# Kernel tuning notes

Measured on AMD Instinct MI355X. Metric: run time of the kernel, lower is better.

The kernel has to match this reference:

```python
import jax, jax.numpy as jnp
import numpy as np

N, F, H, C, CLS = 100000, 128, 4, 32, 2
E = 1600000
NEG_SLOPE = 0.2


def setup_inputs() -> dict:
    key = jax.random.key(0)
    ks = jax.random.split(key, 8)
    x = jax.random.normal(ks[0], (N, F), dtype=jnp.float32)
    edge_index = jax.random.randint(ks[1], (2, E), 0, N, dtype=jnp.int64)
    # GATConv params (PyG layout): lin weight [H*C, F], att vectors [H, C], bias [H*C]
    W_gat = jax.random.normal(ks[2], (H * C, F), dtype=jnp.float32) * (1.0 / np.sqrt(F))
    att_src = jax.random.normal(ks[3], (H, C), dtype=jnp.float32) * (1.0 / np.sqrt(C))
    att_dst = jax.random.normal(ks[4], (H, C), dtype=jnp.float32) * (1.0 / np.sqrt(C))
    b_gat = jnp.zeros((H * C,), dtype=jnp.float32)
    # final classifier Linear(H*C -> CLS)
    W_lin = jax.random.normal(ks[5], (CLS, H * C), dtype=jnp.float32) * (1.0 / np.sqrt(H * C))
    b_lin = jnp.zeros((CLS,), dtype=jnp.float32)
    return {"x": x, "edge_index": edge_index, "W_gat": W_gat, "att_src": att_src,
            "att_dst": att_dst, "b_gat": b_gat, "W_lin": W_lin, "b_lin": b_lin}


def _gat_conv(x, edge_index, W_gat, att_src, att_dst, b_gat):
    # add self loops (PyG default add_self_loops=True)
    loop = jnp.arange(N, dtype=edge_index.dtype)
    src = jnp.concatenate([edge_index[0], loop])  # [E+N]
    dst = jnp.concatenate([edge_index[1], loop])
    h = (x @ W_gat.T).reshape(N, H, C)            # [N, H, C]
    a_src = jnp.einsum('nhc,hc->nh', h, att_src)  # [N, H]
    a_dst = jnp.einsum('nhc,hc->nh', h, att_dst)
    e = a_src[src] + a_dst[dst]                   # [E+N, H]
    e = jnp.where(e >= 0, e, NEG_SLOPE * e)       # leaky_relu(0.2)
    # segment softmax over incoming edges of each destination node
    m = jax.ops.segment_max(e, dst, num_segments=N)          # [N, H]
    ex = jnp.exp(e - m[dst])                                  # [E+N, H]
    denom = jax.ops.segment_sum(ex, dst, num_segments=N)      # [N, H]
    alpha = ex / denom[dst]                                    # [E+N, H]
    msg = alpha[:, :, None] * h[src]                           # [E+N, H, C]
    out = jax.ops.segment_sum(msg, dst, num_segments=N)       # [N, H, C]
    return out.reshape(N, H * C) + b_gat


def reference(x, edge_index, W_gat, att_src, att_dst, b_gat, W_lin, b_lin):
    out = _gat_conv(x, edge_index, W_gat, att_src, att_dst, b_gat)
    out = jax.nn.relu(out)
    return out @ W_lin.T + b_lin  # [N, CLS]
```

## Files before the change

### kernel.cpp

```cpp
#include <hip/hip_runtime.h>

#define NSLOPE  0.2f
#define LEXP(v) __expf((v) >= 0.f ? (v) : NSLOPE * (v))

typedef __attribute__((ext_vector_type(8))) short bf16x8;
typedef __attribute__((ext_vector_type(4))) float f32x4;

__device__ __forceinline__ unsigned bf16_rne(float f) {
    unsigned x = __float_as_uint(f);
    return (x + 0x7fffu + ((x >> 16) & 1u)) >> 16;
}
__device__ __forceinline__ float bf_lo(unsigned u) { return __uint_as_float(u << 16); }
__device__ __forceinline__ float bf_hi(unsigned u) { return __uint_as_float(u & 0xffff0000u); }

__global__ __launch_bounds__(256) void k_gemm_init(
    const float* __restrict__ x, const float* __restrict__ Wg,
    const float* __restrict__ att_src, const float* __restrict__ att_dst,
    unsigned* __restrict__ h2, float* __restrict__ a_src, float* __restrict__ a_dst,
    int N, int* __restrict__ gcur, int nbkt, int cap)
{
    __shared__ unsigned short Wl[128 * 136];
    __shared__ unsigned short wattH[8][128];

    const int t = threadIdx.x;

    if (blockIdx.x >= 512) {
        for (int i = t; i < nbkt; i += 256) gcur[i] = i * cap;
        return;
    }

    for (int i = t; i < 128 * 32; i += 256) {
        int r = i >> 5, c4 = (i & 31) * 4;
        float4 w = *(const float4*)(Wg + r * 128 + c4);
        unsigned* wp = (unsigned*)((char*)Wl + r * 272 + c4 * 2);
        wp[0] = bf16_rne(w.x) | (bf16_rne(w.y) << 16);
        wp[1] = bf16_rne(w.z) | (bf16_rne(w.w) << 16);
    }
    for (int idx = t; idx < 1024; idx += 256) {
        int j = idx >> 7, f = idx & 127;
        const float* av = (j < 4) ? (att_src + j * 32) : (att_dst + (j - 4) * 32);
        int hh = (j & 3) * 32;
        float s = 0.f;
        #pragma unroll 8
        for (int k = 0; k < 32; ++k)
            s += av[k] * Wg[(size_t)(hh + k) * 128 + f];
        wattH[j][f] = (unsigned short)bf16_rne(s);
    }
    __syncthreads();

    const int wave = t >> 6, l = t & 63;
    const int col = l & 15, kg = l >> 4;

    union { bf16x8 v; unsigned short s[8]; } batt[4];
    #pragma unroll
    for (int s4 = 0; s4 < 4; ++s4) {
        #pragma unroll
        for (int jj = 0; jj < 8; ++jj)
            batt[s4].s[jj] = (col < 8) ? wattH[col][s4 * 32 + kg * 8 + jj]
                                       : (unsigned short)0;
    }

    const int nwaves = 512 * 4;
    const int wid = blockIdx.x * 4 + wave;

    for (int mb = wid * 16; mb < N; mb += nwaves * 16) {
        union { bf16x8 v; unsigned u[4]; } af[4];
        int row = mb + col; if (row >= N) row = N - 1;
        const float* xr = x + (size_t)row * 128 + kg * 8;
        #pragma unroll
        for (int s = 0; s < 4; ++s) {
            float4 xa = *(const float4*)(xr + s * 32);
            float4 xb = *(const float4*)(xr + s * 32 + 4);
            af[s].u[0] = bf16_rne(xa.x) | (bf16_rne(xa.y) << 16);
            af[s].u[1] = bf16_rne(xa.z) | (bf16_rne(xa.w) << 16);
            af[s].u[2] = bf16_rne(xb.x) | (bf16_rne(xb.y) << 16);
            af[s].u[3] = bf16_rne(xb.z) | (bf16_rne(xb.w) << 16);
        }

        f32x4 acc[8];
        #pragma unroll
        for (int tl = 0; tl < 8; ++tl) acc[tl] = (f32x4){0.f, 0.f, 0.f, 0.f};
        f32x4 accd = (f32x4){0.f, 0.f, 0.f, 0.f};

        #pragma unroll
        for (int s = 0; s < 4; ++s) {
            #pragma unroll
            for (int tl = 0; tl < 8; ++tl) {
                const bf16x8 bf = *(const bf16x8*)((char*)Wl
                    + (tl * 16 + col) * 272 + (s * 32 + kg * 8) * 2);
                acc[tl] = __builtin_amdgcn_mfma_f32_16x16x32_bf16(af[s].v, bf, acc[tl], 0, 0, 0);
            }
            accd = __builtin_amdgcn_mfma_f32_16x16x32_bf16(af[s].v, batt[s].v, accd, 0, 0, 0);
        }

        #pragma unroll
        for (int tl = 0; tl < 4; ++tl) {
            #pragma unroll
            for (int r = 0; r < 4; ++r) {
                int node = mb + kg * 4 + r;
                if (node < N) {
                    unsigned w = bf16_rne(acc[tl][r]) | (bf16_rne(acc[tl + 4][r]) << 16);
                    h2[(size_t)node * 64 + tl * 16 + col] = w;
                }
            }
        }
        if (col < 8) {
            float* bp = (col < 4) ? a_src : a_dst;
            const int j = col & 3;
            #pragma unroll
            for (int r = 0; r < 4; ++r) {
                int node = mb + kg * 4 + r;
                if (node < N) bp[(size_t)node * 4 + j] = accd[r];
            }
        }
    }
}

__global__ __launch_bounds__(256) void k_partB2(
    const int* __restrict__ ei, int* __restrict__ gcur,
    unsigned* __restrict__ stage, int E, int nbkt, int chunk)
{
    __shared__ int dstc[6272];
    __shared__ int lcnt[1600];
    __shared__ int lbase[1600];
    const int t = threadIdx.x;
    for (int i = t; i < nbkt; i += 256) lcnt[i] = 0;
    __syncthreads();
    const int lo = blockIdx.x * chunk, hi = min(lo + chunk, E);
    for (int e = lo + t; e < hi; e += 256) {
        int d = ei[E + e];
        dstc[e - lo] = d;
        atomicAdd(&lcnt[d >> 6], 1);
    }
    __syncthreads();
    for (int i = t; i < nbkt; i += 256) {
        int c = lcnt[i];
        lbase[i] = (c > 0) ? atomicAdd(&gcur[i], c) : 0;
    }
    __syncthreads();
    for (int e = lo + t; e < hi; e += 256) {
        int s = ei[e];
        int d = dstc[e - lo];
        int pos = atomicAdd(&lbase[d >> 6], 1);
        stage[pos] = (unsigned)s | ((unsigned)(d & 63) << 26);
    }
}

__global__ __launch_bounds__(256) void k_partC(
    const unsigned* __restrict__ stage, const int* __restrict__ gcur,
    const float* __restrict__ a_src, const float* __restrict__ a_dst,
    int2* __restrict__ rowse, int* __restrict__ csr,
    unsigned* __restrict__ alphaE, float* __restrict__ selfa,
    float* __restrict__ invD, int N, int cap)
{
    __shared__ int cnt[64];
    __shared__ int cur[64];
    __shared__ float adl[64][4];
    const int b = blockIdx.x, t = threadIdx.x;
    if (t < 64) {
        cnt[t] = 0;
        int n = (b << 6) + t;
        float4 v = (n < N) ? *(const float4*)(a_dst + (size_t)n * 4)
                           : make_float4(0.f, 0.f, 0.f, 0.f);
        *(float4*)adl[t] = v;
    }
    __syncthreads();
    const int slo = b * cap;
    const int ecnt = gcur[b] - slo;
    for (int e = t; e < ecnt; e += 256)
        atomicAdd(&cnt[stage[slo + e] >> 26], 1);
    __syncthreads();
    int v = 0, pv = 0, c0 = 0;
    if (t < 64) {
        v = cnt[t];
        pv = (v + 7) & ~7;
        int sc = pv;
        #pragma unroll
        for (int m = 1; m < 64; m <<= 1) {
            int u = __shfl_up(sc, m);
            if (t >= m) sc += u;
        }
        c0 = slo + sc - pv;
        cur[t] = c0;
        int n = (b << 6) + t;
        if (n < N) rowse[n] = make_int2(c0, c0 + pv);
    }
    __syncthreads();
    for (int e = t; e < ecnt; e += 256) {
        unsigned u = stage[slo + e];
        int s  = (int)(u & 0x3FFFFFFu);
        int dl = (int)(u >> 26);
        float4 av = *(const float4*)(a_src + (size_t)s * 4);
        float x0 = LEXP(av.x + adl[dl][0]);
        float x1 = LEXP(av.y + adl[dl][1]);
        float x2 = LEXP(av.z + adl[dl][2]);
        float x3 = LEXP(av.w + adl[dl][3]);
        int pos = atomicAdd(&cur[dl], 1);
        csr[pos] = s;
        uint2 pk;
        pk.x = bf16_rne(x0) | (bf16_rne(x2) << 16);
        pk.y = bf16_rne(x1) | (bf16_rne(x3) << 16);
        *(uint2*)(alphaE + (size_t)pos * 2) = pk;
    }
    __syncthreads();
    if (t < 64) {
        int n = (b << 6) + t;
        if (n < N) {
            for (int i = c0 + v; i < c0 + pv; ++i) {
                csr[i] = n;
                *(uint2*)(alphaE + (size_t)i * 2) = make_uint2(0u, 0u);
            }
            float d0 = 0.f, d1 = 0.f, d2 = 0.f, d3 = 0.f;
            for (int i = c0; i < c0 + v; ++i) {
                uint2 pk = *(const uint2*)(alphaE + (size_t)i * 2);
                d0 += bf_lo(pk.x); d2 += bf_hi(pk.x);
                d1 += bf_lo(pk.y); d3 += bf_hi(pk.y);
            }
            float4 av = *(const float4*)(a_src + (size_t)n * 4);
            float p0 = LEXP(av.x + adl[t][0]);
            float p1 = LEXP(av.y + adl[t][1]);
            float p2 = LEXP(av.z + adl[t][2]);
            float p3 = LEXP(av.w + adl[t][3]);
            float i0 = 1.f / (d0 + p0);
            float i1 = 1.f / (d1 + p1);
            float i2 = 1.f / (d2 + p2);
            float i3 = 1.f / (d3 + p3);
            *(float4*)(selfa + (size_t)n * 4) = make_float4(p0 * i0, p1 * i1, p2 * i2, p3 * i3);
            *(float4*)(invD  + (size_t)n * 4) = make_float4(i0, i1, i2, i3);
        }
    }
}

__global__ __launch_bounds__(128) void k_agg(
    const unsigned* __restrict__ h2, const unsigned* __restrict__ aP,
    const float* __restrict__ selfa, const float* __restrict__ invD,
    const int2* __restrict__ rowse, const int* __restrict__ csr,
    const float* __restrict__ b_gat, const float* __restrict__ W_lin,
    const float* __restrict__ b_lin, float* __restrict__ out, int N)
{
    const int t = threadIdx.x;
    const int wave = t >> 6, l = t & 63;
    const int n = blockIdx.x * 2 + wave;
    if (n >= N) return;

    const int m    = l & 31;
    const int half = l >> 5;
    const int c0   = 2 * m;
    const int hsel = m >> 4;
    const unsigned* aPh = aP + hsel;

    const int2 se = rowse[n];
    const int start = se.x, end = se.y;
    const float ivA = invD[n * 4 + hsel];
    const float ivB = invD[n * 4 + 2 + hsel];

    float a00 = 0.f, a01 = 0.f, a10 = 0.f, a11 = 0.f;

    int i = start;
    for (; i + 16 <= end; i += 16) {
        int sk[8]; unsigned d[8]; uint2 u[8];
        #pragma unroll
        for (int k = 0; k < 8; ++k) {
            int j = i + 2 * k + half;
            sk[k] = csr[j];
            d[k]  = aPh[(size_t)j * 2];
        }
        #pragma unroll
        for (int k = 0; k < 8; ++k)
            u[k] = *(const uint2*)(h2 + (size_t)sk[k] * 64 + c0);
        #pragma unroll
        for (int k = 0; k < 8; ++k) {
            float wl = bf_lo(d[k]), wh = bf_hi(d[k]);
            a00 += wl * bf_lo(u[k].x); a01 += wh * bf_hi(u[k].x);
            a10 += wl * bf_lo(u[k].y); a11 += wh * bf_hi(u[k].y);
        }
    }
    if (i < end) {
        int sk[4]; unsigned d[4]; uint2 u[4];
        #pragma unroll
        for (int k = 0; k < 4; ++k) {
            int j = i + 2 * k + half;
            sk[k] = csr[j];
            d[k]  = aPh[(size_t)j * 2];
        }
        #pragma unroll
        for (int k = 0; k < 4; ++k)
            u[k] = *(const uint2*)(h2 + (size_t)sk[k] * 64 + c0);
        #pragma unroll
        for (int k = 0; k < 4; ++k) {
            float wl = bf_lo(d[k]), wh = bf_hi(d[k]);
            a00 += wl * bf_lo(u[k].x); a01 += wh * bf_hi(u[k].x);
            a10 += wl * bf_lo(u[k].y); a11 += wh * bf_hi(u[k].y);
        }
    }

    a00 += __shfl_xor(a00, 32);
    a01 += __shfl_xor(a01, 32);
    a10 += __shfl_xor(a10, 32);
    a11 += __shfl_xor(a11, 32);
    a00 *= ivA; a01 *= ivB; a10 *= ivA; a11 *= ivB;

    {
        uint2 u = *(const uint2*)(h2 + (size_t)n * 64 + c0);
        float sA = selfa[n * 4 + hsel];
        float sB = selfa[n * 4 + 2 + hsel];
        a00 += sA * bf_lo(u.x); a01 += sB * bf_hi(u.x);
        a10 += sA * bf_lo(u.y); a11 += sB * bf_hi(u.y);
    }

    float r0 = fmaxf(a00 + b_gat[c0],      0.f);
    float r1 = fmaxf(a01 + b_gat[c0 + 64], 0.f);
    float r2 = fmaxf(a10 + b_gat[c0 + 1],  0.f);
    float r3 = fmaxf(a11 + b_gat[c0 + 65], 0.f);
    float p0 = r0 * W_lin[c0]       + r1 * W_lin[c0 + 64]
             + r2 * W_lin[c0 + 1]   + r3 * W_lin[c0 + 65];
    float p1 = r0 * W_lin[128 + c0]     + r1 * W_lin[128 + c0 + 64]
             + r2 * W_lin[128 + c0 + 1] + r3 * W_lin[128 + c0 + 65];
    #pragma unroll
    for (int s = 1; s < 32; s <<= 1) {
        p0 += __shfl_xor(p0, s);
        p1 += __shfl_xor(p1, s);
    }
    if (l == 0) {
        out[(size_t)n * 2]     = p0 + b_lin[0];
        out[(size_t)n * 2 + 1] = p1 + b_lin[1];
    }
}

extern "C" void kernel_launch(void* const* d_in, const int* in_sizes, int n_in,
                              void* d_out, int out_size, void* d_ws, size_t ws_size,
                              hipStream_t stream)
{
    const float* x       = (const float*)d_in[0];
    const int*   ei      = (const int*)d_in[1];
    const float* Wg      = (const float*)d_in[2];
    const float* att_src = (const float*)d_in[3];
    const float* att_dst = (const float*)d_in[4];
    const float* b_gat   = (const float*)d_in[5];
    const float* W_lin   = (const float*)d_in[6];
    const float* b_lin   = (const float*)d_in[7];
    float* out = (float*)d_out;

    const int N = in_sizes[0] / 128;
    const int E = in_sizes[1] / 2;
    const int NBKT = (N + 63) >> 6;
    const int CAP  = 1728;
    const int NBLKB = 256;
    const int CHUNK = (E + NBLKB - 1) / NBLKB;

    char* ws = (char*)d_ws;
    unsigned* h2  = (unsigned*)ws;
    float* a_src  = (float*)(h2 + (size_t)N * 64);
    float* a_dst  = a_src + (size_t)N * 4;
    float* selfa  = a_dst + (size_t)N * 4;
    float* invD   = selfa + (size_t)N * 4;
    int2*  rowse  = (int2*)(invD + (size_t)N * 4);
    int*   csr    = (int*)(rowse + N);
    unsigned* alphaE = (unsigned*)(csr + (size_t)NBKT * CAP);
    unsigned* stage  = alphaE + (size_t)NBKT * CAP * 2;
    int*   gcur   = (int*)(stage + (size_t)NBKT * CAP);

    k_gemm_init<<<513, 256, 0, stream>>>(
        x, Wg, att_src, att_dst, h2, a_src, a_dst, N, gcur, NBKT, CAP);
    k_partB2<<<NBLKB, 256, 0, stream>>>(ei, gcur, stage, E, NBKT, CHUNK);
    k_partC<<<NBKT, 256, 0, stream>>>(stage, gcur, a_src, a_dst, rowse, csr,
                                      alphaE, selfa, invD, N, CAP);
    k_agg<<<(N + 1) / 2, 128, 0, stream>>>(h2, alphaE, selfa, invD, rowse, csr,
                                           b_gat, W_lin, b_lin, out, N);
}
```

Before: 164.1 us.

## Fuse CSR build and aggregation into one kernel using LDS-resident edge lists

```diff
diff --git a/kernel.cpp b/kernel.cpp
--- a/kernel.cpp
+++ b/kernel.cpp
@@ -146,17 +146,27 @@
     }
 }
 
-__global__ __launch_bounds__(256) void k_partC(
+__global__ __launch_bounds__(256) void k_aggC(
     const unsigned* __restrict__ stage, const int* __restrict__ gcur,
     const float* __restrict__ a_src, const float* __restrict__ a_dst,
-    int2* __restrict__ rowse, int* __restrict__ csr,
-    unsigned* __restrict__ alphaE, float* __restrict__ selfa,
-    float* __restrict__ invD, int N, int cap)
+    const unsigned* __restrict__ h2, const float* __restrict__ b_gat,
+    const float* __restrict__ W_lin, const float* __restrict__ b_lin,
+    float* __restrict__ out, int N, int cap)
 {
+    __shared__ int      eS[1728];
+    __shared__ unsigned eA0[1728];
+    __shared__ unsigned eA1[1728];
     __shared__ int cnt[64];
     __shared__ int cur[64];
+    __shared__ int rs[64];
+    __shared__ int re[64];
     __shared__ float adl[64][4];
+    __shared__ float selfaL[64][4];
+    __shared__ float invDL[64][4];
+
     const int b = blockIdx.x, t = threadIdx.x;
+    const int wave = t >> 6, l = t & 63;
+
     if (t < 64) {
         cnt[t] = 0;
         int n = (b << 6) + t;
@@ -170,20 +180,18 @@
     for (int e = t; e < ecnt; e += 256)
         atomicAdd(&cnt[stage[slo + e] >> 26], 1);
     __syncthreads();
-    int v = 0, pv = 0, c0 = 0;
     if (t < 64) {
-        v = cnt[t];
-        pv = (v + 7) & ~7;
+        int v = cnt[t];
+        int pv = (v + 7) & ~7;
         int sc = pv;
         #pragma unroll
         for (int m = 1; m < 64; m <<= 1) {
             int u = __shfl_up(sc, m);
             if (t >= m) sc += u;
         }
-        c0 = slo + sc - pv;
+        int c0 = sc - pv;
         cur[t] = c0;
-        int n = (b << 6) + t;
-        if (n < N) rowse[n] = make_int2(c0, c0 + pv);
+        rs[t] = c0; re[t] = c0 + pv;
     }
     __syncthreads();
     for (int e = t; e < ecnt; e += 256) {
@@ -196,25 +204,23 @@
         float x2 = LEXP(av.z + adl[dl][2]);
         float x3 = LEXP(av.w + adl[dl][3]);
         int pos = atomicAdd(&cur[dl], 1);
-        csr[pos] = s;
-        uint2 pk;
-        pk.x = bf16_rne(x0) | (bf16_rne(x2) << 16);
-        pk.y = bf16_rne(x1) | (bf16_rne(x3) << 16);
-        *(uint2*)(alphaE + (size_t)pos * 2) = pk;
+        eS[pos]  = s;
+        eA0[pos] = bf16_rne(x0) | (bf16_rne(x2) << 16);
+        eA1[pos] = bf16_rne(x1) | (bf16_rne(x3) << 16);
     }
     __syncthreads();
     if (t < 64) {
         int n = (b << 6) + t;
         if (n < N) {
-            for (int i = c0 + v; i < c0 + pv; ++i) {
-                csr[i] = n;
-                *(uint2*)(alphaE + (size_t)i * 2) = make_uint2(0u, 0u);
+            const int c0 = rs[t], e1 = cur[t], pe = re[t];
+            for (int i = e1; i < pe; ++i) {
+                eS[i] = n; eA0[i] = 0u; eA1[i] = 0u;
             }
             float d0 = 0.f, d1 = 0.f, d2 = 0.f, d3 = 0.f;
-            for (int i = c0; i < c0 + v; ++i) {
-                uint2 pk = *(const uint2*)(alphaE + (size_t)i * 2);
-                d0 += bf_lo(pk.x); d2 += bf_hi(pk.x);
-                d1 += bf_lo(pk.y); d3 += bf_hi(pk.y);
+            for (int i = c0; i < e1; ++i) {
+                unsigned p0 = eA0[i], p1 = eA1[i];
+                d0 += bf_lo(p0); d2 += bf_hi(p0);
+                d1 += bf_lo(p1); d3 += bf_hi(p1);
             }
             float4 av = *(const float4*)(a_src + (size_t)n * 4);
             float p0 = LEXP(av.x + adl[t][0]);
@@ -225,105 +231,95 @@
             float i1 = 1.f / (d1 + p1);
             float i2 = 1.f / (d2 + p2);
             float i3 = 1.f / (d3 + p3);
-            *(float4*)(selfa + (size_t)n * 4) = make_float4(p0 * i0, p1 * i1, p2 * i2, p3 * i3);
-            *(float4*)(invD  + (size_t)n * 4) = make_float4(i0, i1, i2, i3);
-        }
-    }
-}
-
-__global__ __launch_bounds__(128) void k_agg(
-    const unsigned* __restrict__ h2, const unsigned* __restrict__ aP,
-    const float* __restrict__ selfa, const float* __restrict__ invD,
-    const int2* __restrict__ rowse, const int* __restrict__ csr,
-    const float* __restrict__ b_gat, const float* __restrict__ W_lin,
-    const float* __restrict__ b_lin, float* __restrict__ out, int N)
-{
-    const int t = threadIdx.x;
-    const int wave = t >> 6, l = t & 63;
-    const int n = blockIdx.x * 2 + wave;
-    if (n >= N) return;
+            selfaL[t][0] = p0 * i0; selfaL[t][1] = p1 * i1;
+            selfaL[t][2] = p2 * i2; selfaL[t][3] = p3 * i3;
+            invDL[t][0] = i0; invDL[t][1] = i1;
+            invDL[t][2] = i2; invDL[t][3] = i3;
+        }
+    }
+    __syncthreads();
 
     const int m    = l & 31;
     const int half = l >> 5;
-    const int c0   = 2 * m;
+    const int cch  = 2 * m;
     const int hsel = m >> 4;
-    const unsigned* aPh = aP + hsel;
-
-    const int2 se = rowse[n];
-    const int start = se.x, end = se.y;
-    const float ivA = invD[n * 4 + hsel];
-    const float ivB = invD[n * 4 + 2 + hsel];
-
-    float a00 = 0.f, a01 = 0.f, a10 = 0.f, a11 = 0.f;
-
-    int i = start;
-    for (; i + 16 <= end; i += 16) {
-        int sk[8]; unsigned d[8]; uint2 u[8];
-        #pragma unroll
-        for (int k = 0; k < 8; ++k) {
-            int j = i + 2 * k + half;
-            sk[k] = csr[j];
-            d[k]  = aPh[(size_t)j * 2];
-        }
-        #pragma unroll
-        for (int k = 0; k < 8; ++k)
-            u[k] = *(const uint2*)(h2 + (size_t)sk[k] * 64 + c0);
-        #pragma unroll
-        for (int k = 0; k < 8; ++k) {
-            float wl = bf_lo(d[k]), wh = bf_hi(d[k]);
-            a00 += wl * bf_lo(u[k].x); a01 += wh * bf_hi(u[k].x);
-            a10 += wl * bf_lo(u[k].y); a11 += wh * bf_hi(u[k].y);
-        }
-    }
-    if (i < end) {
-        int sk[4]; unsigned d[4]; uint2 u[4];
-        #pragma unroll
-        for (int k = 0; k < 4; ++k) {
-            int j = i + 2 * k + half;
-            sk[k] = csr[j];
-            d[k]  = aPh[(size_t)j * 2];
-        }
-        #pragma unroll
-        for (int k = 0; k < 4; ++k)
-            u[k] = *(const uint2*)(h2 + (size_t)sk[k] * 64 + c0);
-        #pragma unroll
-        for (int k = 0; k < 4; ++k) {
-            float wl = bf_lo(d[k]), wh = bf_hi(d[k]);
-            a00 += wl * bf_lo(u[k].x); a01 += wh * bf_hi(u[k].x);
-            a10 += wl * bf_lo(u[k].y); a11 += wh * bf_hi(u[k].y);
-        }
-    }
-
-    a00 += __shfl_xor(a00, 32);
-    a01 += __shfl_xor(a01, 32);
-    a10 += __shfl_xor(a10, 32);
-    a11 += __shfl_xor(a11, 32);
-    a00 *= ivA; a01 *= ivB; a10 *= ivA; a11 *= ivB;
-
-    {
-        uint2 u = *(const uint2*)(h2 + (size_t)n * 64 + c0);
-        float sA = selfa[n * 4 + hsel];
-        float sB = selfa[n * 4 + 2 + hsel];
-        a00 += sA * bf_lo(u.x); a01 += sB * bf_hi(u.x);
-        a10 += sA * bf_lo(u.y); a11 += sB * bf_hi(u.y);
-    }
-
-    float r0 = fmaxf(a00 + b_gat[c0],      0.f);
-    float r1 = fmaxf(a01 + b_gat[c0 + 64], 0.f);
-    float r2 = fmaxf(a10 + b_gat[c0 + 1],  0.f);
-    float r3 = fmaxf(a11 + b_gat[c0 + 65], 0.f);
-    float p0 = r0 * W_lin[c0]       + r1 * W_lin[c0 + 64]
-             + r2 * W_lin[c0 + 1]   + r3 * W_lin[c0 + 65];
-    float p1 = r0 * W_lin[128 + c0]     + r1 * W_lin[128 + c0 + 64]
-             + r2 * W_lin[128 + c0 + 1] + r3 * W_lin[128 + c0 + 65];
-    #pragma unroll
-    for (int s = 1; s < 32; s <<= 1) {
-        p0 += __shfl_xor(p0, s);
-        p1 += __shfl_xor(p1, s);
-    }
-    if (l == 0) {
-        out[(size_t)n * 2]     = p0 + b_lin[0];
-        out[(size_t)n * 2 + 1] = p1 + b_lin[1];
+    const unsigned* eAh = hsel ? eA1 : eA0;
+
+    for (int ln = wave; ln < 64; ln += 4) {
+        int n = (b << 6) + ln;
+        if (n >= N) break;
+        const int start = rs[ln], end = re[ln];
+        float a00 = 0.f, a01 = 0.f, a10 = 0.f, a11 = 0.f;
+
+        int i = start;
+        for (; i + 16 <= end; i += 16) {
+            int sk[8]; unsigned d[8]; uint2 u[8];
+            #pragma unroll
+            for (int k = 0; k < 8; ++k) {
+                int j = i + 2 * k + half;
+                sk[k] = eS[j];
+                d[k]  = eAh[j];
+            }
+            #pragma unroll
+            for (int k = 0; k < 8; ++k)
+                u[k] = *(const uint2*)(h2 + (size_t)sk[k] * 64 + cch);
+            #pragma unroll
+            for (int k = 0; k < 8; ++k) {
+                float wl = bf_lo(d[k]), wh = bf_hi(d[k]);
+                a00 += wl * bf_lo(u[k].x); a01 += wh * bf_hi(u[k].x);
+                a10 += wl * bf_lo(u[k].y); a11 += wh * bf_hi(u[k].y);
+            }
+        }
+        if (i < end) {
+            int sk[4]; unsigned d[4]; uint2 u[4];
+            #pragma unroll
+            for (int k = 0; k < 4; ++k) {
+                int j = i + 2 * k + half;
+                sk[k] = eS[j];
+                d[k]  = eAh[j];
+            }
+            #pragma unroll
+            for (int k = 0; k < 4; ++k)
+                u[k] = *(const uint2*)(h2 + (size_t)sk[k] * 64 + cch);
+            #pragma unroll
+            for (int k = 0; k < 4; ++k) {
+                float wl = bf_lo(d[k]), wh = bf_hi(d[k]);
+                a00 += wl * bf_lo(u[k].x); a01 += wh * bf_hi(u[k].x);
+                a10 += wl * bf_lo(u[k].y); a11 += wh * bf_hi(u[k].y);
+            }
+        }
+
+        a00 += __shfl_xor(a00, 32);
+        a01 += __shfl_xor(a01, 32);
+        a10 += __shfl_xor(a10, 32);
+        a11 += __shfl_xor(a11, 32);
+        const float ivA = invDL[ln][hsel], ivB = invDL[ln][2 + hsel];
+        a00 *= ivA; a01 *= ivB; a10 *= ivA; a11 *= ivB;
+
+        {
+            uint2 u = *(const uint2*)(h2 + (size_t)n * 64 + cch);
+            float sA = selfaL[ln][hsel], sB = selfaL[ln][2 + hsel];
+            a00 += sA * bf_lo(u.x); a01 += sB * bf_hi(u.x);
+            a10 += sA * bf_lo(u.y); a11 += sB * bf_hi(u.y);
+        }
+
+        float r0 = fmaxf(a00 + b_gat[cch],      0.f);
+        float r1 = fmaxf(a01 + b_gat[cch + 64], 0.f);
+        float r2 = fmaxf(a10 + b_gat[cch + 1],  0.f);
+        float r3 = fmaxf(a11 + b_gat[cch + 65], 0.f);
+        float p0 = r0 * W_lin[cch]       + r1 * W_lin[cch + 64]
+                 + r2 * W_lin[cch + 1]   + r3 * W_lin[cch + 65];
+        float p1 = r0 * W_lin[128 + cch]     + r1 * W_lin[128 + cch + 64]
+                 + r2 * W_lin[128 + cch + 1] + r3 * W_lin[128 + cch + 65];
+        #pragma unroll
+        for (int s = 1; s < 32; s <<= 1) {
+            p0 += __shfl_xor(p0, s);
+            p1 += __shfl_xor(p1, s);
+        }
+        if (l == 0) {
+            out[(size_t)n * 2]     = p0 + b_lin[0];
+            out[(size_t)n * 2 + 1] = p1 + b_lin[1];
+        }
     }
 }
 
@@ -352,19 +348,12 @@
     unsigned* h2  = (unsigned*)ws;
     float* a_src  = (float*)(h2 + (size_t)N * 64);
     float* a_dst  = a_src + (size_t)N * 4;
-    float* selfa  = a_dst + (size_t)N * 4;
-    float* invD   = selfa + (size_t)N * 4;
-    int2*  rowse  = (int2*)(invD + (size_t)N * 4);
-    int*   csr    = (int*)(rowse + N);
-    unsigned* alphaE = (unsigned*)(csr + (size_t)NBKT * CAP);
-    unsigned* stage  = alphaE + (size_t)NBKT * CAP * 2;
+    unsigned* stage = (unsigned*)(a_dst + (size_t)N * 4);
     int*   gcur   = (int*)(stage + (size_t)NBKT * CAP);
 
     k_gemm_init<<<513, 256, 0, stream>>>(
         x, Wg, att_src, att_dst, h2, a_src, a_dst, N, gcur, NBKT, CAP);
     k_partB2<<<NBLKB, 256, 0, stream>>>(ei, gcur, stage, E, NBKT, CHUNK);
-    k_partC<<<NBKT, 256, 0, stream>>>(stage, gcur, a_src, a_dst, rowse, csr,
-                                      alphaE, selfa, invD, N, CAP);
-    k_agg<<<(N + 1) / 2, 128, 0, stream>>>(h2, alphaE, selfa, invD, rowse, csr,
-                                           b_gat, W_lin, b_lin, out, N);
-}
+    k_aggC<<<NBKT, 256, 0, stream>>>(stage, gcur, a_src, a_dst, h2,
+                                     b_gat, W_lin, b_lin, out, N, CAP);
+}
```

New measurement: 142.0 us. 1.16x faster.
